# Optimization experiments

Measured on AMD Instinct MI355X. Metric: run time of the kernel, lower is better.

The kernel has to match this reference:

```python
import jax, jax.numpy as jnp
import numpy as np

HIDDEN = 512
HEADS = 8
PREFIX = 1  # prefix_size: rows >= PREFIX may not attend to cols < PREFIX (except causal tril already zeroed those only partially)


def setup_inputs() -> dict:
    key = jax.random.key(0)
    k1, k2, k3 = jax.random.split(key, 3)
    B, L, D = 2, 4096, HIDDEN
    x = jax.random.normal(k1, (B, L, D), dtype=jnp.float32)
    # torch Linear(hidden, 3*hidden): y = x @ W^T + b; we store W^T directly as [D, 3D]
    w_in = jax.random.normal(k2, (D, 3 * D), dtype=jnp.float32) * (1.0 / np.sqrt(D))
    b_in = jnp.zeros((3 * D,), dtype=jnp.float32)
    w_out = jax.random.normal(k3, (D, D), dtype=jnp.float32) * (1.0 / np.sqrt(D))
    b_out = jnp.zeros((D,), dtype=jnp.float32)
    return {"x": x, "w_in": w_in, "b_in": b_in, "w_out": w_out, "b_out": b_out}


def _prefix_causal_mask(L):
    # tril(ones) then zero out [prefix:, :prefix]
    m = jnp.tril(jnp.ones((L, L), dtype=bool))
    m = m.at[PREFIX:, :PREFIX].set(False)
    return m  # True = attend allowed


def reference(x, w_in, b_in, w_out, b_out):
    B, L, D = x.shape
    H, hd = HEADS, D // HEADS
    qkv = x @ w_in + b_in  # [B, L, 3D]
    q, k, v = jnp.split(qkv, 3, axis=-1)
    q = q.reshape(B, L, H, hd).transpose(0, 2, 1, 3)  # [B,H,L,hd]
    k = k.reshape(B, L, H, hd).transpose(0, 2, 1, 3)
    v = v.reshape(B, L, H, hd).transpose(0, 2, 1, 3)
    scale = 1.0 / np.sqrt(hd).astype(np.float32)
    attn = jnp.einsum('bhqd,bhkd->bhqk', q, k) * scale  # [B,H,L,L]
    mask = _prefix_causal_mask(L)
    attn = jnp.where(mask[None, None, :, :], attn, -jnp.inf)
    attn = jax.nn.softmax(attn, axis=-1)  # dropout p=0.0 -> identity
    out = jnp.einsum('bhqk,bhkd->bhqd', attn, v)  # [B,H,L,hd]
    out = out.transpose(0, 2, 1, 3).reshape(B, L, D)
    return out @ w_out + b_out
```

## Files before the change

kernel.cpp:

```cpp
#include <hip/hip_runtime.h>
#include <hip/hip_bf16.h>

#define BSZ   2
#define LSEQ  4096
#define DH    512
#define NH    8
#define HDIM  64

typedef unsigned short ushort_t;
typedef __attribute__((ext_vector_type(8))) short s8v;
typedef __attribute__((ext_vector_type(4))) float f4v;

__device__ __forceinline__ ushort_t f2bf(float f) {
    __hip_bfloat16 h = __float2bfloat16(f);
    return *(ushort_t*)&h;
}

__device__ __forceinline__ void gld_lds16(const ushort_t* g, ushort_t* l) {
    __builtin_amdgcn_global_load_lds(
        (const __attribute__((address_space(1))) void*)g,
        (__attribute__((address_space(3))) void*)l, 16, 0, 0);
}

__global__ __launch_bounds__(256) void cast_bf16(const float* __restrict__ src,
                                                 ushort_t* __restrict__ dst, int n)
{
    int i = (blockIdx.x * 256 + threadIdx.x) * 4;
    if (i + 3 < n) {
        float4 v = *(const float4*)&src[i];
        ushort_t o[4] = {f2bf(v.x), f2bf(v.y), f2bf(v.z), f2bf(v.w)};
        *(uint2*)&dst[i] = *(uint2*)o;
    }
}

__global__ __launch_bounds__(256) void transpose_cast(const float* __restrict__ src,
                                                      ushort_t* __restrict__ dst,
                                                      int R, int C)
{
    __shared__ float tile[32][33];
    int r0 = blockIdx.y * 32, c0 = blockIdx.x * 32;
    int t = threadIdx.x;
    int tr = t >> 5, tc = t & 31;
    #pragma unroll
    for (int i = 0; i < 4; i++)
        tile[tr + 8 * i][tc] = src[(size_t)(r0 + tr + 8 * i) * C + c0 + tc];
    __syncthreads();
    #pragma unroll
    for (int i = 0; i < 4; i++) {
        int oc = tr + 8 * i;
        dst[(size_t)(c0 + oc) * R + r0 + tc] = f2bf(tile[tc][oc]);
    }
}

__global__ __launch_bounds__(256) void vtrans(const ushort_t* __restrict__ qkv,
                                              ushort_t* __restrict__ vt)
{
    __shared__ ushort_t T[64][72];
    const int lt = blockIdx.x, h = blockIdx.y, b = blockIdx.z;
    const int l0 = lt * 64;
    const int t = threadIdx.x;
    {
        int r = t >> 2, c = (t & 3) * 16;
        size_t g = ((size_t)(b * LSEQ + l0 + r)) * (3 * DH) + 2 * DH + h * HDIM + c;
        *(uint4*)&T[r][c]     = *(const uint4*)&qkv[g];
        *(uint4*)&T[r][c + 8] = *(const uint4*)&qkv[g + 8];
    }
    __syncthreads();
    {
        int d = t >> 2, cl = (t & 3) * 16;
        ushort_t tmp[16];
        #pragma unroll
        for (int j = 0; j < 16; j++) tmp[j] = T[cl + j][d];
        size_t g = ((size_t)((b * NH + h) * 64 + d)) * LSEQ + l0 + cl;
        *(uint4*)&vt[g]     = *(uint4*)&tmp[0];
        *(uint4*)&vt[g + 8] = *(uint4*)&tmp[8];
    }
}

template <typename OUT>
__global__ __launch_bounds__(256) void gemm_bt(const ushort_t* __restrict__ A,
                                               const ushort_t* __restrict__ Bt,
                                               const float* __restrict__ bias,
                                               OUT* __restrict__ C,
                                               int M, int N, int K)
{
    __shared__ ushort_t As[128 * 32];
    __shared__ ushort_t Bs[128 * 32];
    const int tid = threadIdx.x;
    const int row0 = blockIdx.y * 128, col0 = blockIdx.x * 128;
    const int wid = tid >> 6, lane = tid & 63;
    const int wm = wid >> 1, wn = wid & 1;
    const int quad = lane >> 4, ln = lane & 15;

    f4v acc[4][4] = {};

    const int srow = (lane >> 2);
    const int scol = (lane & 3) * 8;

    for (int k0 = 0; k0 < K; k0 += 32) {
        #pragma unroll
        for (int t = 0; t < 2; t++) {
            int chunk = wid * 2 + t;
            int r = chunk * 16 + srow;
            gld_lds16(&A[(size_t)(row0 + r) * K + k0 + scol], &As[chunk * 512]);
            gld_lds16(&Bt[(size_t)(col0 + r) * K + k0 + scol], &Bs[chunk * 512]);
        }
        __syncthreads();
        s8v af[4], bf[4];
        #pragma unroll
        for (int mt = 0; mt < 4; mt++)
            af[mt] = *(const s8v*)&As[(wm * 64 + mt * 16 + ln) * 32 + quad * 8];
        #pragma unroll
        for (int nt = 0; nt < 4; nt++)
            bf[nt] = *(const s8v*)&Bs[(wn * 64 + nt * 16 + ln) * 32 + quad * 8];
        #pragma unroll
        for (int mt = 0; mt < 4; mt++)
            #pragma unroll
            for (int nt = 0; nt < 4; nt++)
                acc[mt][nt] = __builtin_amdgcn_mfma_f32_16x16x32_bf16(
                    af[mt], bf[nt], acc[mt][nt], 0, 0, 0);
        __syncthreads();
    }

    #pragma unroll
    for (int mt = 0; mt < 4; mt++) {
        #pragma unroll
        for (int nt = 0; nt < 4; nt++) {
            int c = col0 + wn * 64 + nt * 16 + ln;
            float bv = bias[c];
            #pragma unroll
            for (int reg = 0; reg < 4; reg++) {
                int r = row0 + wm * 64 + mt * 16 + quad * 4 + reg;
                float v = acc[mt][nt][reg] + bv;
                if constexpr (sizeof(OUT) == 2)
                    C[(size_t)r * N + c] = (OUT)f2bf(v);
                else
                    C[(size_t)r * N + c] = v;
            }
        }
    }
}

__global__ __launch_bounds__(128) void flash_mfma(const ushort_t* __restrict__ qkv,
                                                  const ushort_t* __restrict__ vt,
                                                  ushort_t* __restrict__ att)
{
    __shared__ ushort_t Ks[64 * 72];
    __shared__ ushort_t Vs[64 * 72];
    __shared__ ushort_t Ps[32 * 72];

    const int p  = blockIdx.x >> 1;
    const int qh = blockIdx.x & 1;
    const int h = blockIdx.y, b = blockIdx.z;
    const int tid = threadIdx.x;
    const int w = tid >> 6, lane = tid & 63;
    const int quad = lane >> 4, ln = lane & 15;

    const int sr = tid >> 1, sc = (tid & 1) * 32;
    const int ldsw = sr * 72 + sc;
    const size_t kstep = (size_t)64 * 3 * DH;
    const float C_EXP = 0.18033688011112042f;

    const int qts[2] = {63 - p, p};

    for (int ti = 0; ti < 2; ti++) {
        const int qt = qts[ti], q0 = qt * 64;
        const int qrow0 = q0 + qh * 32 + w * 16;

        const ushort_t* qrow = qkv + ((size_t)(b * LSEQ + qrow0 + ln)) * (3 * DH) + h * HDIM;
        s8v qa0 = *(const s8v*)(qrow + quad * 8);
        s8v qa1 = *(const s8v*)(qrow + 32 + quad * 8);

        float l_s = 0.0f;
        f4v o_acc[4] = {};

        size_t gk = ((size_t)(b * LSEQ + sr)) * (3 * DH) + DH + h * HDIM + sc;
        size_t gv = ((size_t)((b * NH + h) * 64 + sr)) * LSEQ + sc;
        uint4 pk0 = *(const uint4*)&qkv[gk];
        uint4 pk1 = *(const uint4*)&qkv[gk + 8];
        uint4 pk2 = *(const uint4*)&qkv[gk + 16];
        uint4 pk3 = *(const uint4*)&qkv[gk + 24];
        uint4 pv0 = *(const uint4*)&vt[gv];
        uint4 pv1 = *(const uint4*)&vt[gv + 8];
        uint4 pv2 = *(const uint4*)&vt[gv + 16];
        uint4 pv3 = *(const uint4*)&vt[gv + 24];

        const int prow = (w * 16 + ln) * 72;

        for (int kt = 0; kt <= qt; kt++) {
            const int k0 = kt * 64;
            __syncthreads();
            *(uint4*)&Ks[ldsw]      = pk0;
            *(uint4*)&Ks[ldsw + 8]  = pk1;
            *(uint4*)&Ks[ldsw + 16] = pk2;
            *(uint4*)&Ks[ldsw + 24] = pk3;
            *(uint4*)&Vs[ldsw]      = pv0;
            *(uint4*)&Vs[ldsw + 8]  = pv1;
            *(uint4*)&Vs[ldsw + 16] = pv2;
            *(uint4*)&Vs[ldsw + 24] = pv3;
            if (kt < qt) {
                gk += kstep; gv += 64;
                pk0 = *(const uint4*)&qkv[gk];
                pk1 = *(const uint4*)&qkv[gk + 8];
                pk2 = *(const uint4*)&qkv[gk + 16];
                pk3 = *(const uint4*)&qkv[gk + 24];
                pv0 = *(const uint4*)&vt[gv];
                pv1 = *(const uint4*)&vt[gv + 8];
                pv2 = *(const uint4*)&vt[gv + 16];
                pv3 = *(const uint4*)&vt[gv + 24];
            }
            __syncthreads();

            f4v s[4] = {};
            #pragma unroll
            for (int nt = 0; nt < 4; nt++) {
                s8v kb0 = *(const s8v*)&Ks[(nt * 16 + ln) * 72 + quad * 8];
                s8v kb1 = *(const s8v*)&Ks[(nt * 16 + ln) * 72 + 32 + quad * 8];
                s[nt] = __builtin_amdgcn_mfma_f32_16x16x32_bf16(kb0, qa0, s[nt], 0, 0, 0);
                s[nt] = __builtin_amdgcn_mfma_f32_16x16x32_bf16(kb1, qa1, s[nt], 0, 0, 0);
            }

            float pp[4][4];
            const int q = qrow0 + ln;
            if (kt == qt) {
                #pragma unroll
                for (int nt = 0; nt < 4; nt++) {
                    #pragma unroll
                    for (int reg = 0; reg < 4; reg++) {
                        int kidx = k0 + nt * 16 + quad * 4 + reg;
                        bool valid = (kidx <= q) && (kidx >= 1 || q == 0);
                        pp[nt][reg] = valid ? __builtin_amdgcn_exp2f(s[nt][reg] * C_EXP) : 0.0f;
                    }
                }
            } else {
                #pragma unroll
                for (int nt = 0; nt < 4; nt++)
                    #pragma unroll
                    for (int reg = 0; reg < 4; reg++)
                        pp[nt][reg] = __builtin_amdgcn_exp2f(s[nt][reg] * C_EXP);
                if (kt == 0 && quad == 0)
                    pp[0][0] = 0.0f;
            }

            #pragma unroll
            for (int nt = 0; nt < 4; nt++)
                l_s += (pp[nt][0] + pp[nt][1]) + (pp[nt][2] + pp[nt][3]);

            #pragma unroll
            for (int nt = 0; nt < 4; nt++) {
                unsigned int lo = (unsigned int)f2bf(pp[nt][0]) | ((unsigned int)f2bf(pp[nt][1]) << 16);
                unsigned int hi = (unsigned int)f2bf(pp[nt][2]) | ((unsigned int)f2bf(pp[nt][3]) << 16);
                uint2 pkd; pkd.x = lo; pkd.y = hi;
                *(uint2*)&Ps[prow + nt * 16 + quad * 4] = pkd;
            }

            s8v pa0 = *(const s8v*)&Ps[prow + quad * 8];
            s8v pa1 = *(const s8v*)&Ps[prow + 32 + quad * 8];
            #pragma unroll
            for (int dt = 0; dt < 4; dt++) {
                s8v vb0 = *(const s8v*)&Vs[(dt * 16 + ln) * 72 + quad * 8];
                s8v vb1 = *(const s8v*)&Vs[(dt * 16 + ln) * 72 + 32 + quad * 8];
                o_acc[dt] = __builtin_amdgcn_mfma_f32_16x16x32_bf16(pa0, vb0, o_acc[dt], 0, 0, 0);
                o_acc[dt] = __builtin_amdgcn_mfma_f32_16x16x32_bf16(pa1, vb1, o_acc[dt], 0, 0, 0);
            }
        }

        float lf = l_s;
        lf += __shfl_xor(lf, 16);
        lf += __shfl_xor(lf, 32);
        #pragma unroll
        for (int reg = 0; reg < 4; reg++) {
            float linv = 1.0f / __shfl(lf, quad * 4 + reg);
            size_t r = (size_t)(b * LSEQ + qrow0 + quad * 4 + reg);
            #pragma unroll
            for (int dt = 0; dt < 4; dt++)
                att[r * DH + h * HDIM + dt * 16 + ln] = f2bf(o_acc[dt][reg] * linv);
        }
    }
}

extern "C" void kernel_launch(void* const* d_in, const int* in_sizes, int n_in,
                              void* d_out, int out_size, void* d_ws, size_t ws_size,
                              hipStream_t stream)
{
    const float* x     = (const float*)d_in[0];
    const float* w_in  = (const float*)d_in[1];
    const float* b_in  = (const float*)d_in[2];
    const float* w_out = (const float*)d_in[3];
    const float* b_out = (const float*)d_in[4];
    float* out = (float*)d_out;

    const int M = BSZ * LSEQ;
    char* ws = (char*)d_ws;
    ushort_t* xb    = (ushort_t*)ws;                       ws += (size_t)M * DH * 2;
    ushort_t* w_inT = (ushort_t*)ws;                       ws += (size_t)3 * DH * DH * 2;
    ushort_t* w_outT= (ushort_t*)ws;                       ws += (size_t)DH * DH * 2;
    ushort_t* qkvb  = (ushort_t*)ws;                       ws += (size_t)M * 3 * DH * 2;
    ushort_t* vtb   = (ushort_t*)ws;                       ws += (size_t)M * DH * 2;
    ushort_t* attb  = (ushort_t*)ws;

    cast_bf16<<<(M * DH / 4 + 255) / 256, 256, 0, stream>>>(x, xb, M * DH);
    transpose_cast<<<dim3(3 * DH / 32, DH / 32), 256, 0, stream>>>(w_in, w_inT, DH, 3 * DH);
    transpose_cast<<<dim3(DH / 32, DH / 32), 256, 0, stream>>>(w_out, w_outT, DH, DH);

    gemm_bt<ushort_t><<<dim3(3 * DH / 128, M / 128), 256, 0, stream>>>(
        xb, w_inT, b_in, qkvb, M, 3 * DH, DH);

    vtrans<<<dim3(LSEQ / 64, NH, BSZ), 256, 0, stream>>>(qkvb, vtb);

    flash_mfma<<<dim3(64, NH, BSZ), 128, 0, stream>>>(qkvb, vtb, attb);

    gemm_bt<float><<<dim3(DH / 128, M / 128), 256, 0, stream>>>(
        attb, w_outT, b_out, out, M, DH, DH);
}
```

Measured before the change: 209.4 us.

## Process full 64-row query tile per attention block and fuse prep casts into one kernel

```diff
diff --git a/kernel.cpp b/kernel.cpp
--- a/kernel.cpp
+++ b/kernel.cpp
@@ -22,23 +22,12 @@
         (__attribute__((address_space(3))) void*)l, 16, 0, 0);
 }
 
-__global__ __launch_bounds__(256) void cast_bf16(const float* __restrict__ src,
-                                                 ushort_t* __restrict__ dst, int n)
-{
-    int i = (blockIdx.x * 256 + threadIdx.x) * 4;
-    if (i + 3 < n) {
-        float4 v = *(const float4*)&src[i];
-        ushort_t o[4] = {f2bf(v.x), f2bf(v.y), f2bf(v.z), f2bf(v.w)};
-        *(uint2*)&dst[i] = *(uint2*)o;
-    }
-}
-
-__global__ __launch_bounds__(256) void transpose_cast(const float* __restrict__ src,
-                                                      ushort_t* __restrict__ dst,
-                                                      int R, int C)
+__device__ __forceinline__ void transpose_tile(const float* __restrict__ src,
+                                               ushort_t* __restrict__ dst,
+                                               int R, int C, int bx, int by)
 {
     __shared__ float tile[32][33];
-    int r0 = blockIdx.y * 32, c0 = blockIdx.x * 32;
+    int r0 = by * 32, c0 = bx * 32;
     int t = threadIdx.x;
     int tr = t >> 5, tc = t & 31;
     #pragma unroll
@@ -52,6 +41,28 @@
     }
 }
 
+__global__ __launch_bounds__(256) void prep(const float* __restrict__ x,
+                                            ushort_t* __restrict__ xb,
+                                            const float* __restrict__ w_in,
+                                            ushort_t* __restrict__ w_inT,
+                                            const float* __restrict__ w_out,
+                                            ushort_t* __restrict__ w_outT)
+{
+    int bx = blockIdx.x;
+    if (bx < 4096) {
+        int i = (bx * 256 + threadIdx.x) * 4;
+        float4 v = *(const float4*)&x[i];
+        ushort_t o[4] = {f2bf(v.x), f2bf(v.y), f2bf(v.z), f2bf(v.w)};
+        *(uint2*)&xb[i] = *(uint2*)o;
+    } else if (bx < 4864) {
+        int idx = bx - 4096;
+        transpose_tile(w_in, w_inT, DH, 3 * DH, idx % 48, idx / 48);
+    } else {
+        int idx = bx - 4864;
+        transpose_tile(w_out, w_outT, DH, DH, idx % 16, idx / 16);
+    }
+}
+
 __global__ __launch_bounds__(256) void vtrans(const ushort_t* __restrict__ qkv,
                                               ushort_t* __restrict__ vt)
 {
@@ -147,10 +158,9 @@
 {
     __shared__ ushort_t Ks[64 * 72];
     __shared__ ushort_t Vs[64 * 72];
-    __shared__ ushort_t Ps[32 * 72];
-
-    const int p  = blockIdx.x >> 1;
-    const int qh = blockIdx.x & 1;
+    __shared__ ushort_t Ps[64 * 72];
+
+    const int p = blockIdx.x;
     const int h = blockIdx.y, b = blockIdx.z;
     const int tid = threadIdx.x;
     const int w = tid >> 6, lane = tid & 63;
@@ -165,14 +175,19 @@
 
     for (int ti = 0; ti < 2; ti++) {
         const int qt = qts[ti], q0 = qt * 64;
-        const int qrow0 = q0 + qh * 32 + w * 16;
-
-        const ushort_t* qrow = qkv + ((size_t)(b * LSEQ + qrow0 + ln)) * (3 * DH) + h * HDIM;
-        s8v qa0 = *(const s8v*)(qrow + quad * 8);
-        s8v qa1 = *(const s8v*)(qrow + 32 + quad * 8);
-
-        float l_s = 0.0f;
-        f4v o_acc[4] = {};
+        const int qrow0 = q0 + w * 32;
+
+        s8v qa[2][2];
+        #pragma unroll
+        for (int qg = 0; qg < 2; qg++) {
+            const ushort_t* qrow = qkv
+                + ((size_t)(b * LSEQ + qrow0 + qg * 16 + ln)) * (3 * DH) + h * HDIM;
+            qa[qg][0] = *(const s8v*)(qrow + quad * 8);
+            qa[qg][1] = *(const s8v*)(qrow + 32 + quad * 8);
+        }
+
+        float l_s[2] = {0.0f, 0.0f};
+        f4v o_acc[2][4] = {};
 
         size_t gk = ((size_t)(b * LSEQ + sr)) * (3 * DH) + DH + h * HDIM + sc;
         size_t gv = ((size_t)((b * NH + h) * 64 + sr)) * LSEQ + sc;
@@ -184,8 +199,6 @@
         uint4 pv1 = *(const uint4*)&vt[gv + 8];
         uint4 pv2 = *(const uint4*)&vt[gv + 16];
         uint4 pv3 = *(const uint4*)&vt[gv + 24];
-
-        const int prow = (w * 16 + ln) * 72;
 
         for (int kt = 0; kt <= qt; kt++) {
             const int k0 = kt * 64;
@@ -211,70 +224,85 @@
             }
             __syncthreads();
 
-            f4v s[4] = {};
+            s8v kb[4][2], vb[4][2];
             #pragma unroll
             for (int nt = 0; nt < 4; nt++) {
-                s8v kb0 = *(const s8v*)&Ks[(nt * 16 + ln) * 72 + quad * 8];
-                s8v kb1 = *(const s8v*)&Ks[(nt * 16 + ln) * 72 + 32 + quad * 8];
-                s[nt] = __builtin_amdgcn_mfma_f32_16x16x32_bf16(kb0, qa0, s[nt], 0, 0, 0);
-                s[nt] = __builtin_amdgcn_mfma_f32_16x16x32_bf16(kb1, qa1, s[nt], 0, 0, 0);
-            }
-
-            float pp[4][4];
-            const int q = qrow0 + ln;
-            if (kt == qt) {
+                kb[nt][0] = *(const s8v*)&Ks[(nt * 16 + ln) * 72 + quad * 8];
+                kb[nt][1] = *(const s8v*)&Ks[(nt * 16 + ln) * 72 + 32 + quad * 8];
+            }
+            #pragma unroll
+            for (int dt = 0; dt < 4; dt++) {
+                vb[dt][0] = *(const s8v*)&Vs[(dt * 16 + ln) * 72 + quad * 8];
+                vb[dt][1] = *(const s8v*)&Vs[(dt * 16 + ln) * 72 + 32 + quad * 8];
+            }
+
+            #pragma unroll
+            for (int qg = 0; qg < 2; qg++) {
+                f4v s[4] = {};
                 #pragma unroll
                 for (int nt = 0; nt < 4; nt++) {
+                    s[nt] = __builtin_amdgcn_mfma_f32_16x16x32_bf16(kb[nt][0], qa[qg][0], s[nt], 0, 0, 0);
+                    s[nt] = __builtin_amdgcn_mfma_f32_16x16x32_bf16(kb[nt][1], qa[qg][1], s[nt], 0, 0, 0);
+                }
+
+                float pp[4][4];
+                const int q = qrow0 + qg * 16 + ln;
+                if (kt == qt) {
                     #pragma unroll
-                    for (int reg = 0; reg < 4; reg++) {
-                        int kidx = k0 + nt * 16 + quad * 4 + reg;
-                        bool valid = (kidx <= q) && (kidx >= 1 || q == 0);
-                        pp[nt][reg] = valid ? __builtin_amdgcn_exp2f(s[nt][reg] * C_EXP) : 0.0f;
+                    for (int nt = 0; nt < 4; nt++) {
+                        #pragma unroll
+                        for (int reg = 0; reg < 4; reg++) {
+                            int kidx = k0 + nt * 16 + quad * 4 + reg;
+                            bool valid = (kidx <= q) && (kidx >= 1 || q == 0);
+                            pp[nt][reg] = valid ? __builtin_amdgcn_exp2f(s[nt][reg] * C_EXP) : 0.0f;
+                        }
                     }
+                } else {
+                    #pragma unroll
+                    for (int nt = 0; nt < 4; nt++)
+                        #pragma unroll
+                        for (int reg = 0; reg < 4; reg++)
+                            pp[nt][reg] = __builtin_amdgcn_exp2f(s[nt][reg] * C_EXP);
+                    if (kt == 0 && quad == 0)
+                        pp[0][0] = 0.0f;
                 }
-            } else {
+
                 #pragma unroll
                 for (int nt = 0; nt < 4; nt++)
-                    #pragma unroll
-                    for (int reg = 0; reg < 4; reg++)
-                        pp[nt][reg] = __builtin_amdgcn_exp2f(s[nt][reg] * C_EXP);
-                if (kt == 0 && quad == 0)
-                    pp[0][0] = 0.0f;
-            }
-
-            #pragma unroll
-            for (int nt = 0; nt < 4; nt++)
-                l_s += (pp[nt][0] + pp[nt][1]) + (pp[nt][2] + pp[nt][3]);
-
-            #pragma unroll
-            for (int nt = 0; nt < 4; nt++) {
-                unsigned int lo = (unsigned int)f2bf(pp[nt][0]) | ((unsigned int)f2bf(pp[nt][1]) << 16);
-                unsigned int hi = (unsigned int)f2bf(pp[nt][2]) | ((unsigned int)f2bf(pp[nt][3]) << 16);
-                uint2 pkd; pkd.x = lo; pkd.y = hi;
-                *(uint2*)&Ps[prow + nt * 16 + quad * 4] = pkd;
-            }
-
-            s8v pa0 = *(const s8v*)&Ps[prow + quad * 8];
-            s8v pa1 = *(const s8v*)&Ps[prow + 32 + quad * 8];
-            #pragma unroll
-            for (int dt = 0; dt < 4; dt++) {
-                s8v vb0 = *(const s8v*)&Vs[(dt * 16 + ln) * 72 + quad * 8];
-                s8v vb1 = *(const s8v*)&Vs[(dt * 16 + ln) * 72 + 32 + quad * 8];
-                o_acc[dt] = __builtin_amdgcn_mfma_f32_16x16x32_bf16(pa0, vb0, o_acc[dt], 0, 0, 0);
-                o_acc[dt] = __builtin_amdgcn_mfma_f32_16x16x32_bf16(pa1, vb1, o_acc[dt], 0, 0, 0);
-            }
-        }
-
-        float lf = l_s;
-        lf += __shfl_xor(lf, 16);
-        lf += __shfl_xor(lf, 32);
-        #pragma unroll
-        for (int reg = 0; reg < 4; reg++) {
-            float linv = 1.0f / __shfl(lf, quad * 4 + reg);
-            size_t r = (size_t)(b * LSEQ + qrow0 + quad * 4 + reg);
-            #pragma unroll
-            for (int dt = 0; dt < 4; dt++)
-                att[r * DH + h * HDIM + dt * 16 + ln] = f2bf(o_acc[dt][reg] * linv);
+                    l_s[qg] += (pp[nt][0] + pp[nt][1]) + (pp[nt][2] + pp[nt][3]);
+
+                const int prow = (w * 32 + qg * 16 + ln) * 72;
+                #pragma unroll
+                for (int nt = 0; nt < 4; nt++) {
+                    unsigned int lo = (unsigned int)f2bf(pp[nt][0]) | ((unsigned int)f2bf(pp[nt][1]) << 16);
+                    unsigned int hi = (unsigned int)f2bf(pp[nt][2]) | ((unsigned int)f2bf(pp[nt][3]) << 16);
+                    uint2 pkd; pkd.x = lo; pkd.y = hi;
+                    *(uint2*)&Ps[prow + nt * 16 + quad * 4] = pkd;
+                }
+
+                s8v pa0 = *(const s8v*)&Ps[prow + quad * 8];
+                s8v pa1 = *(const s8v*)&Ps[prow + 32 + quad * 8];
+                #pragma unroll
+                for (int dt = 0; dt < 4; dt++) {
+                    o_acc[qg][dt] = __builtin_amdgcn_mfma_f32_16x16x32_bf16(pa0, vb[dt][0], o_acc[qg][dt], 0, 0, 0);
+                    o_acc[qg][dt] = __builtin_amdgcn_mfma_f32_16x16x32_bf16(pa1, vb[dt][1], o_acc[qg][dt], 0, 0, 0);
+                }
+            }
+        }
+
+        #pragma unroll
+        for (int qg = 0; qg < 2; qg++) {
+            float lf = l_s[qg];
+            lf += __shfl_xor(lf, 16);
+            lf += __shfl_xor(lf, 32);
+            #pragma unroll
+            for (int reg = 0; reg < 4; reg++) {
+                float linv = 1.0f / __shfl(lf, quad * 4 + reg);
+                size_t r = (size_t)(b * LSEQ + qrow0 + qg * 16 + quad * 4 + reg);
+                #pragma unroll
+                for (int dt = 0; dt < 4; dt++)
+                    att[r * DH + h * HDIM + dt * 16 + ln] = f2bf(o_acc[qg][dt][reg] * linv);
+            }
         }
     }
 }
@@ -299,16 +327,14 @@
     ushort_t* vtb   = (ushort_t*)ws;                       ws += (size_t)M * DH * 2;
     ushort_t* attb  = (ushort_t*)ws;
 
-    cast_bf16<<<(M * DH / 4 + 255) / 256, 256, 0, stream>>>(x, xb, M * DH);
-    transpose_cast<<<dim3(3 * DH / 32, DH / 32), 256, 0, stream>>>(w_in, w_inT, DH, 3 * DH);
-    transpose_cast<<<dim3(DH / 32, DH / 32), 256, 0, stream>>>(w_out, w_outT, DH, DH);
+    prep<<<5120, 256, 0, stream>>>(x, xb, w_in, w_inT, w_out, w_outT);
 
     gemm_bt<ushort_t><<<dim3(3 * DH / 128, M / 128), 256, 0, stream>>>(
         xb, w_inT, b_in, qkvb, M, 3 * DH, DH);
 
     vtrans<<<dim3(LSEQ / 64, NH, BSZ), 256, 0, stream>>>(qkvb, vtb);
 
-    flash_mfma<<<dim3(64, NH, BSZ), 128, 0, stream>>>(qkvb, vtb, attb);
+    flash_mfma<<<dim3(32, NH, BSZ), 128, 0, stream>>>(qkvb, vtb, attb);
 
     gemm_bt<float><<<dim3(DH / 128, M / 128), 256, 0, stream>>>(
         attb, w_outT, b_out, out, M, DH, DH);
```

New measurement: 211.3 us. Within noise of the previous version (+0.9%).
